# Performance work log

Hardware: AMD Instinct MI355X
Metric: run time of the kernel (lower is better)

Reference implementation:

```python
import jax, jax.numpy as jnp
import numpy as np
from jax import lax

B, T, D, U = 64, 512, 1024, 1024
INIT_SCALE = 0.05  # keras 'uniform' initializer: U(-0.05, 0.05)


def setup_inputs() -> dict:
    key = jax.random.key(0)
    kx, kw, ku = jax.random.split(key, 3)
    x = jax.random.normal(kx, (B, T, D), dtype=jnp.float32)
    kernel = jax.random.uniform(kw, (D, U), dtype=jnp.float32,
                                minval=-INIT_SCALE, maxval=INIT_SCALE)
    recurrent_kernel = jax.random.uniform(ku, (U, U), dtype=jnp.float32,
                                          minval=-INIT_SCALE, maxval=INIT_SCALE)
    return {"x": x, "kernel": kernel, "recurrent_kernel": recurrent_kernel}


def reference(x, kernel, recurrent_kernel):
    # h_t = x_t @ W + h_{t-1} @ U, h_0 = 0; return last h (return_sequences=False)
    # Precompute the input projection for all timesteps in one big GEMM.
    xs = jnp.einsum('btd,du->btu', x, kernel)          # [B, T, U]
    h0 = jnp.zeros((x.shape[0], recurrent_kernel.shape[0]), dtype=x.dtype)

    def step(h, xt):
        h = xt + h @ recurrent_kernel                   # [B, U]
        return h, None

    h_last, _ = lax.scan(step, h0, jnp.swapaxes(xs, 0, 1))  # scan over T
    return h_last                                       # [B, U]
```

## Files before the change

### kernel.cpp

```cpp
#include <hip/hip_runtime.h>
#include <hip/hip_bf16.h>

typedef __attribute__((ext_vector_type(4))) float f32x4;
typedef __attribute__((ext_vector_type(8))) short bf16x8;
typedef __attribute__((ext_vector_type(4))) short s16x4;

#define SLOT (1024 * 1024)

__device__ __forceinline__ short f2bfs(float f) {
  __hip_bfloat16 h = __float2bfloat16(f);
  union { __hip_bfloat16 h; short s; } u; u.h = h;
  return u.s;
}
__device__ __forceinline__ float bf2fs(short s) {
  union { unsigned u; float f; } v; v.u = ((unsigned)(unsigned short)s) << 16;
  return v.f;
}

__device__ __forceinline__ void gload16(void* l, const void* g) {
  __builtin_amdgcn_global_load_lds(
      (const __attribute__((address_space(1))) unsigned int*)g,
      (__attribute__((address_space(3))) unsigned int*)l, 16, 0, 0);
}

template<int RM>
__device__ __forceinline__ int rmap(int R) {
  return (RM == 0) ? R
       : (RM == 3) ? (((R & 63) << 9) | ((R >> 6) << 2))
                   : (((R >> 6) << 7) | (R & 63));
}

template<int ADD, int OUT>
__device__ __forceinline__ void epi128(
    f32x4 (&acc)[4][4], void* __restrict__ Cp, int ldc,
    const short* __restrict__ AddP,
    int row0, int col0, int M, int wave, int lane) {
  const int wm = wave >> 1, wn = wave & 1;
  const int l16 = lane & 15;
  #pragma unroll
  for (int m = 0; m < 4; ++m) {
    #pragma unroll
    for (int n = 0; n < 4; ++n) {
      const int grow0 = row0 + wm * 64 + m * 16 + ((lane >> 4) << 2);
      const int gcol  = col0 + wn * 64 + n * 16 + l16;
      #pragma unroll
      for (int r = 0; r < 4; ++r) {
        const int R = grow0 + r;
        if (R < M) {
          float val = acc[m][n][r];
          if (ADD == 2) {
            int ar = (((R >> 6) << 7) | (R & 63)) + 64;
            val += bf2fs(AddP[(size_t)ar * 1024 + gcol]);
          }
          if (OUT == 0) ((short*)Cp)[(size_t)R * ldc + gcol] = f2bfs(val);
          else          ((float*)Cp)[(size_t)R * ldc + gcol] = val;
        }
      }
    }
  }
}

struct TileAddr {
  const short *a0, *a1, *b0, *b1;
  int dA0, dA1, dB0, dB1;
  int offA[4], offB[4];
};
template<int RM>
__device__ __forceinline__ TileAddr mk_addr(
    const short* A, int lda, const short* BT, int ldb,
    int row0, int col0, int tid, int wave, int lane) {
  TileAddr t;
  const int wm = wave >> 1, wn = wave & 1;
  const int l16 = lane & 15, kg = lane >> 4;
  const int r0 = tid >> 2, g0 = tid & 3;
  const int gs0 = g0 ^ ((r0 >> 1) & 3);
  const int r1 = r0 + 64;
  const int gs1 = g0 ^ ((r1 >> 1) & 3);
  t.a0 = A + (size_t)rmap<RM>(row0 + r0) * lda + gs0 * 8;
  t.a1 = A + (size_t)rmap<RM>(row0 + r1) * lda + gs1 * 8;
  t.b0 = BT + (size_t)(col0 + r0) * ldb + gs0 * 8;
  t.b1 = BT + (size_t)(col0 + r1) * ldb + gs1 * 8;
  t.dA0 = tid * 16; t.dA1 = t.dA0 + 4096;
  t.dB0 = 8192 + tid * 16; t.dB1 = t.dB0 + 4096;
  #pragma unroll
  for (int m = 0; m < 4; ++m) {
    int row = wm * 64 + m * 16 + l16;
    t.offA[m] = (row * 4 + (kg ^ ((row >> 1) & 3))) * 16;
  }
  #pragma unroll
  for (int n = 0; n < 4; ++n) {
    int c = wn * 64 + n * 16 + l16;
    t.offB[n] = 8192 + (c * 4 + (kg ^ ((c >> 1) & 3))) * 16;
  }
  return t;
}
__device__ __forceinline__ void stage_to(const TileAddr& ta, char* buf, int ko) {
  gload16(buf + ta.dA0, ta.a0 + ko); gload16(buf + ta.dA1, ta.a1 + ko);
  gload16(buf + ta.dB0, ta.b0 + ko); gload16(buf + ta.dB1, ta.b1 + ko);
}
__device__ __forceinline__ void compute_step(
    const TileAddr& ta, const char* buf, f32x4 (&acc)[4][4]) {
  bf16x8 af[4], bfr[4];
  #pragma unroll
  for (int m = 0; m < 4; ++m) af[m] = *(const bf16x8*)(buf + ta.offA[m]);
  #pragma unroll
  for (int n = 0; n < 4; ++n) bfr[n] = *(const bf16x8*)(buf + ta.offB[n]);
  __builtin_amdgcn_s_setprio(1);
  #pragma unroll
  for (int m = 0; m < 4; ++m)
    #pragma unroll
    for (int n = 0; n < 4; ++n)
      acc[m][n] = __builtin_amdgcn_mfma_f32_16x16x32_bf16(af[m], bfr[n], acc[m][n], 0, 0, 0);
  __builtin_amdgcn_s_setprio(0);
}
template<int RM>
__device__ __forceinline__ void gemm128_d4(
    char* lds, f32x4 (&acc)[4][4],
    const short* __restrict__ A, int lda,
    const short* __restrict__ BT, int ldb,
    int row0, int col0, int nkt, int tid, int wave, int lane) {
  TileAddr ta = mk_addr<RM>(A, lda, BT, ldb, row0, col0, tid, wave, lane);
  #pragma unroll
  for (int p = 0; p < 4; ++p)
    stage_to(ta, lds + p * 16384, p * 32);
  int bufc = 0, bufn = 4;
  for (int t = 0; t < nkt; ++t) {
    const int w = nkt - 1 - t;
    if (w >= 3)      { asm volatile("s_waitcnt vmcnt(12)" ::: "memory"); }
    else if (w == 2) { asm volatile("s_waitcnt vmcnt(8)" ::: "memory"); }
    else if (w == 1) { asm volatile("s_waitcnt vmcnt(4)" ::: "memory"); }
    else             { asm volatile("s_waitcnt vmcnt(0)" ::: "memory"); }
    __builtin_amdgcn_s_barrier();
    asm volatile("" ::: "memory");
    if (t + 4 < nkt) stage_to(ta, lds + bufn * 16384, (t + 4) * 32);
    compute_step(ta, lds + bufc * 16384, acc);
    bufc = (bufc == 4) ? 0 : bufc + 1;
    bufn = (bufn == 4) ? 0 : bufn + 1;
  }
}
__device__ __forceinline__ void run_unit_d4(char* lds,
    const short* A, const short* BT, short* C, int ldc,
    int tile, int tid, int wave, int lane) {
  f32x4 acc[4][4] = {};
  int row0 = (tile >> 3) * 128, col0 = (tile & 7) * 128;
  gemm128_d4<0>(lds, acc, A, 1024, BT, 1024, row0, col0, 32, tid, wave, lane);
  epi128<0, 0>(acc, C, ldc, nullptr, row0, col0, 1024, wave, lane);
}

template<int RM>
__device__ __forceinline__ void gemm8ph(
    char* lds, f32x4 (&acc)[4][4],
    const short* __restrict__ A, int lda,
    const short* __restrict__ BT, int ldb,
    int row0, int col0, int nkt, int tid, int wave, int lane) {
  const int wm = wave >> 1, wn = wave & 1;
  const int l16 = lane & 15, kg = (lane >> 4) & 3;

  const short* aP[2][2];
  #pragma unroll
  for (int l = 0; l < 2; ++l) {
    int G = l * 512 + tid;
    int rp = G >> 3, gs = (G & 7) ^ (rp & 7);
    #pragma unroll
    for (int h = 0; h < 2; ++h)
      aP[l][h] = A + (size_t)rmap<RM>(row0 + h * 128 + rp) * lda + gs * 8;
  }
  const short* bP[2];
  {
    int rp = tid >> 3, gs = (tid & 7) ^ (rp & 7);
    #pragma unroll
    for (int h = 0; h < 2; ++h)
      bP[h] = BT + (size_t)(col0 + h * 64 + rp) * ldb + gs * 8;
  }

  int offA[4][2], offB[4][2];
  #pragma unroll
  for (int m = 0; m < 4; ++m) {
    int rp = (wm & 1) * 64 + m * 16 + l16;
    #pragma unroll
    for (int ks = 0; ks < 2; ++ks) {
      int gsrc = ks * 4 + kg;
      offA[m][ks] = (wm >> 1) * 16384 + (rp * 8 + (gsrc ^ (rp & 7))) * 16;
    }
  }
  #pragma unroll
  for (int n = 0; n < 4; ++n) {
    int rp = n * 16 + l16;
    #pragma unroll
    for (int ks = 0; ks < 2; ++ks) {
      int gsrc = ks * 4 + kg;
      offB[n][ks] = wn * 8192 + (rp * 8 + (gsrc ^ (rp & 7))) * 16;
    }
  }

  auto SA = [&](int kt, int ad_t, int h) {
    char* dst = lds + ad_t * 32768 + h * 16384 + tid * 16;
    gload16(dst,        aP[0][h] + kt * 64);
    gload16(dst + 8192, aP[1][h] + kt * 64);
  };
  auto SB = [&](int kt, int h) {
    gload16(lds + 98304 + (kt & 1) * 16384 + h * 8192 + tid * 16,
            bP[h] + kt * 64);
  };

  SA(0, 0, 0); SA(0, 0, 1);
  SB(0, 0); SB(0, 1);
  SA(1, 1, 0); SA(1, 1, 1);
  SB(1, 0); SB(1, 1);

  bf16x8 bR[4][2];
  int ad = 0;
  for (int kt = 0; kt < nkt; ++kt) {
    char* baseA = lds + ad * 32768;
    char* baseB = lds + 98304 + (kt & 1) * 16384;
    const int ad2 = (ad >= 1) ? ad - 1 : 2;
    if (kt == nkt - 1) { asm volatile("s_waitcnt vmcnt(0)" ::: "memory"); }
    else               { asm volatile("s_waitcnt vmcnt(6)" ::: "memory"); }
    __builtin_amdgcn_s_barrier();
    __builtin_amdgcn_sched_barrier(0);
    {
      #pragma unroll
      for (int n = 0; n < 4; ++n)
        #pragma unroll
        for (int ks = 0; ks < 2; ++ks)
          bR[n][ks] = *(const bf16x8*)(baseB + offB[n][ks]);
      bf16x8 aR[2][2];
      #pragma unroll
      for (int mm = 0; mm < 2; ++mm)
        #pragma unroll
        for (int ks = 0; ks < 2; ++ks)
          aR[mm][ks] = *(const bf16x8*)(baseA + offA[mm][ks]);
      if (kt + 2 < nkt) { SA(kt + 2, ad2, 0); SA(kt + 2, ad2, 1); }
      __builtin_amdgcn_s_setprio(1);
      #pragma unroll
      for (int mm = 0; mm < 2; ++mm)
        #pragma unroll
        for (int n = 0; n < 4; ++n)
          #pragma unroll
          for (int ks = 0; ks < 2; ++ks)
            acc[mm][n] = __builtin_amdgcn_mfma_f32_16x16x32_bf16(
                aR[mm][ks], bR[n][ks], acc[mm][n], 0, 0, 0);
      __builtin_amdgcn_s_setprio(0);
    }
    __builtin_amdgcn_s_barrier();
    __builtin_amdgcn_sched_barrier(0);
    {
      bf16x8 aR[2][2];
      #pragma unroll
      for (int mm = 0; mm < 2; ++mm)
        #pragma unroll
        for (int ks = 0; ks < 2; ++ks)
          aR[mm][ks] = *(const bf16x8*)(baseA + offA[2 + mm][ks]);
      if (kt + 2 < nkt) { SB(kt + 2, 0); SB(kt + 2, 1); }
      __builtin_amdgcn_s_setprio(1);
      #pragma unroll
      for (int mm = 0; mm < 2; ++mm)
        #pragma unroll
        for (int n = 0; n < 4; ++n)
          #pragma unroll
          for (int ks = 0; ks < 2; ++ks)
            acc[2 + mm][n] = __builtin_amdgcn_mfma_f32_16x16x32_bf16(
                aR[mm][ks], bR[n][ks], acc[2 + mm][n], 0, 0, 0);
      __builtin_amdgcn_s_setprio(0);
    }
    ad = (ad == 2) ? 0 : ad + 1;
  }
}

__device__ __forceinline__ void run_unit8(char* lds,
    const short* A, const short* BT, short* C, int ldc,
    int tile, int tid, int wave, int lane) {
  f32x4 acc[4][4] = {};
  int row0 = (tile >> 3) * 256, col0 = (tile & 7) * 128;
  gemm8ph<0>(lds, acc, A, 1024, BT, 1024, row0, col0, 16, tid, wave, lane);
  epi128<0, 0>(acc, C, ldc, nullptr, row0, col0, 1024, wave, lane);
}


__global__ __launch_bounds__(256) void k_prep(
    const float* __restrict__ W, const float* __restrict__ Uf,
    const float* __restrict__ X,
    short* __restrict__ BTcat, short* __restrict__ slab, short* __restrict__ XB) {
  __shared__ float tf[32][36];
  int b = blockIdx.x, t = threadIdx.x;
  if (b < 2048) {
    const float* src = (b < 1024) ? W : Uf;
    int bb = b & 1023;
    int i0 = (bb >> 5) * 32, j0 = (bb & 31) * 32;
    int r = t >> 3, c = (t & 7) * 4;
    *(f32x4*)&tf[r][c] = *(const f32x4*)(src + (size_t)(i0 + r) * 1024 + j0 + c);
    __syncthreads();
    s16x4 o;
    o.x = f2bfs(tf[c + 0][r]); o.y = f2bfs(tf[c + 1][r]);
    o.z = f2bfs(tf[c + 2][r]); o.w = f2bfs(tf[c + 3][r]);
    if (b < 1024)
      *(s16x4*)(BTcat + (size_t)(j0 + r) * 4096 + 3072 + i0 + c) = o;
    else
      *(s16x4*)(slab + (size_t)(j0 + r) * 1024 + i0 + c) = o;
  } else if (b < 3072) {
    int q = b - 2048;
    const float* src = (q < 512) ? Uf : W;
    short* dst = slab + (size_t)((q < 512) ? 9 : 17) * SLOT;
    int qq = q & 511;
    size_t base = (size_t)qq * 2048 + (size_t)t * 8;
    f32x4 a = *(const f32x4*)(src + base);
    f32x4 c2 = *(const f32x4*)(src + base + 4);
    bf16x8 o;
    o[0] = f2bfs(a.x);  o[1] = f2bfs(a.y);  o[2] = f2bfs(a.z);  o[3] = f2bfs(a.w);
    o[4] = f2bfs(c2.x); o[5] = f2bfs(c2.y); o[6] = f2bfs(c2.z); o[7] = f2bfs(c2.w);
    *(bf16x8*)(dst + base) = o;
  } else {
    int q = b - 3072;
    size_t base = ((size_t)q * 256 + t) * 32;
    #pragma unroll
    for (int i = 0; i < 4; ++i) {
      f32x4 a = *(const f32x4*)(X + base + i * 8);
      f32x4 c2 = *(const f32x4*)(X + base + i * 8 + 4);
      bf16x8 o;
      o[0] = f2bfs(a.x);  o[1] = f2bfs(a.y);  o[2] = f2bfs(a.z);  o[3] = f2bfs(a.w);
      o[4] = f2bfs(c2.x); o[5] = f2bfs(c2.y); o[6] = f2bfs(c2.z); o[7] = f2bfs(c2.w);
      *(bf16x8*)(XB + base + i * 8) = o;
    }
  }
}

__global__ __launch_bounds__(512) void k_pre1(short* slab, short* BTcat) {
  __shared__ __align__(16) char lds[131072];
  int tid = threadIdx.x, wave = tid >> 6, lane = tid & 63;
  int b = blockIdx.x, u = b >> 5, q = b & 31;
  short* s = slab;
  if (u == 0)
    run_unit8(lds, s, s + (size_t)9 * SLOT, s + (size_t)1 * SLOT, 1024, q, tid, wave, lane);
  else if (u == 1)
    run_unit8(lds, s + (size_t)9 * SLOT, s, s + (size_t)10 * SLOT, 1024, q, tid, wave, lane);
  else if (u == 2)
    run_unit8(lds, s, s + (size_t)17 * SLOT, BTcat + 2048, 4096, q, tid, wave, lane);
  else
    run_unit8(lds, s + (size_t)17 * SLOT, s, s + (size_t)16 * SLOT, 1024, q, tid, wave, lane);
}

__global__ __launch_bounds__(512) void k_pre2(short* slab, short* BTcat) {
  __shared__ __align__(16) char lds[131072];
  int tid = threadIdx.x, wave = tid >> 6, lane = tid & 63;
  int b = blockIdx.x, u = b >> 5, q = b & 31;
  short* s = slab;
  if (u == 0)
    run_unit8(lds, s + (size_t)1 * SLOT, s + (size_t)17 * SLOT, BTcat + 1024, 4096, q, tid, wave, lane);
  else if (u == 1)
    run_unit8(lds, s + (size_t)1 * SLOT, s + (size_t)16 * SLOT, BTcat, 4096, q, tid, wave, lane);
  else if (u == 2)
    run_unit8(lds, s + (size_t)1 * SLOT, s + (size_t)10 * SLOT, s + (size_t)2 * SLOT, 1024, q, tid, wave, lane);
  else
    run_unit8(lds, s + (size_t)10 * SLOT, s + (size_t)1 * SLOT, s + (size_t)11 * SLOT, 1024, q, tid, wave, lane);
}

__global__ __launch_bounds__(512) void k_big(
    const short* __restrict__ XB, const short* __restrict__ BTcat,
    short* __restrict__ FA) {
  __shared__ __align__(16) char lds[131072];
  int tid = threadIdx.x, wave = tid >> 6, lane = tid & 63;
  int c = blockIdx.x;
  int c2 = (c & 7) * 32 + (c >> 3);
  f32x4 acc[4][4] = {};
  int row0 = (c2 >> 3) * 256, col0 = (c2 & 7) * 128;
  gemm8ph<3>(lds, acc, XB, 1024, BTcat, 4096, row0, col0, 64, tid, wave, lane);
  epi128<0, 0>(acc, FA, 1024, nullptr, row0, col0, 8192, wave, lane);
}

template<int OUT>
__global__ __launch_bounds__(256) void k_lvl(
    const short* __restrict__ Fin, const short* __restrict__ PT,
    void* __restrict__ Fout, int M, int nComb,
    const short* __restrict__ sA0, const short* __restrict__ sB0, short* __restrict__ sC0,
    const short* __restrict__ sA1, const short* __restrict__ sB1, short* __restrict__ sC1) {
  __shared__ __align__(16) char lds[81920];
  int tid = threadIdx.x, wave = tid >> 6, lane = tid & 63;
  int b = blockIdx.x;
  if (b < nComb) {
    f32x4 acc[4][4] = {};
    int row0 = (b >> 3) * 128, col0 = (b & 7) * 128;
    gemm128_d4<2>(lds, acc, Fin, 1024, PT, 1024, row0, col0, 32, tid, wave, lane);
    epi128<2, OUT>(acc, Fout, 1024, Fin, row0, col0, M, wave, lane);
  } else {
    int q = b - nComb;
    const short* sa = (q < 64) ? sA0 : sA1;
    const short* sb = (q < 64) ? sB0 : sB1;
    short* sc = (q < 64) ? sC0 : sC1;
    run_unit_d4(lds, sa, sb, sc, 1024, q & 63, tid, wave, lane);
  }
}

extern "C" void kernel_launch(void* const* d_in, const int* in_sizes, int n_in,
                              void* d_out, int out_size, void* d_ws, size_t ws_size,
                              hipStream_t stream) {
  const float* X = (const float*)d_in[0];
  const float* W = (const float*)d_in[1];
  const float* U = (const float*)d_in[2];
  float* outp = (float*)d_out;

  char* ws = (char*)d_ws;
  short* XB    = (short*)ws;
  short* FB    = (short*)ws;
  short* BTcat = (short*)(ws + ((size_t)64 << 20));
  short* slab  = (short*)(ws + ((size_t)72 << 20));
  short* FA    = (short*)(ws + ((size_t)108 << 20));
  auto sl = [&](int i) { return slab + (size_t)i * SLOT; };

  k_prep<<<7168, 256, 0, stream>>>(W, U, X, BTcat, slab, XB);
  k_pre1<<<128, 512, 0, stream>>>(slab, BTcat);
  k_pre2<<<128, 512, 0, stream>>>(slab, BTcat);
  k_big<<<256, 512, 0, stream>>>(XB, BTcat, FA);

  k_lvl<0><<<384, 256, 0, stream>>>(FA, sl(2), FB, 4096, 256,
                                    sl(2), sl(11), sl(3), sl(11), sl(2), sl(12));
  k_lvl<0><<<256, 256, 0, stream>>>(FB, sl(3), FA, 2048, 128,
                                    sl(3), sl(12), sl(4), sl(12), sl(3), sl(13));
  k_lvl<0><<<192, 256, 0, stream>>>(FA, sl(4), FB, 1024, 64,
                                    sl(4), sl(13), sl(5), sl(13), sl(4), sl(14));
  k_lvl<0><<<160, 256, 0, stream>>>(FB, sl(5), FA, 512, 32,
                                    sl(5), sl(14), sl(6), sl(14), sl(5), sl(15));
  k_lvl<0><<<144, 256, 0, stream>>>(FA, sl(6), FB, 256, 16,
                                    sl(6), sl(15), sl(7), sl(15), sl(6), sl(16));
  k_lvl<0><<<72, 256, 0, stream>>>(FB, sl(7), FA, 128, 8,
                                   sl(7), sl(16), sl(8), nullptr, nullptr, nullptr);
  k_lvl<1><<<8, 256, 0, stream>>>(FA, sl(8), outp, 64, 8,
                                  nullptr, nullptr, nullptr, nullptr, nullptr, nullptr);
}
```

Baseline: 320.0 us.

## Overlap X bf16 conversion with small weight-power GEMMs in fused kernels

Takes the fp32-to-bf16 conversion of the large input X out of the prep kernel. It splits that work across the two small precompute GEMM launches, which before used only 128 workgroups. Extra workgroups in each launch now convert half of X, so the bandwidth-bound conversion runs beside the compute-bound weight-power GEMMs. The cost is a heavier launch of 2176 blocks, each needing 128KB of LDS because the GEMM and convert blocks share one kernel. This can limit how many convert blocks fit per CU and can delay the GEMM blocks.

```diff
diff --git a/kernel.cpp b/kernel.cpp
--- a/kernel.cpp
+++ b/kernel.cpp
@@ -277,10 +277,9 @@
 }
 
 
-__global__ __launch_bounds__(256) void k_prep(
+__global__ __launch_bounds__(256) void k_prep_tc(
     const float* __restrict__ W, const float* __restrict__ Uf,
-    const float* __restrict__ X,
-    short* __restrict__ BTcat, short* __restrict__ slab, short* __restrict__ XB) {
+    short* __restrict__ BTcat, short* __restrict__ slab) {
   __shared__ float tf[32][36];
   int b = blockIdx.x, t = threadIdx.x;
   if (b < 2048) {
@@ -297,7 +296,7 @@
       *(s16x4*)(BTcat + (size_t)(j0 + r) * 4096 + 3072 + i0 + c) = o;
     else
       *(s16x4*)(slab + (size_t)(j0 + r) * 1024 + i0 + c) = o;
-  } else if (b < 3072) {
+  } else {
     int q = b - 2048;
     const float* src = (q < 512) ? Uf : W;
     short* dst = slab + (size_t)((q < 512) ? 9 : 17) * SLOT;
@@ -309,49 +308,50 @@
     o[0] = f2bfs(a.x);  o[1] = f2bfs(a.y);  o[2] = f2bfs(a.z);  o[3] = f2bfs(a.w);
     o[4] = f2bfs(c2.x); o[5] = f2bfs(c2.y); o[6] = f2bfs(c2.z); o[7] = f2bfs(c2.w);
     *(bf16x8*)(dst + base) = o;
+  }
+}
+
+template<int PH>
+__global__ __launch_bounds__(512) void k_fuse(
+    const float* __restrict__ X, short* __restrict__ XB,
+    short* slab, short* BTcat) {
+  __shared__ __align__(16) char lds[131072];
+  int tid = threadIdx.x;
+  int b = blockIdx.x;
+  short* s = slab;
+  if (b < 128) {
+    int wave = tid >> 6, lane = tid & 63;
+    int u = b >> 5, q = b & 31;
+    if (PH == 0) {
+      if (u == 0)
+        run_unit8(lds, s, s + (size_t)9 * SLOT, s + (size_t)1 * SLOT, 1024, q, tid, wave, lane);
+      else if (u == 1)
+        run_unit8(lds, s + (size_t)9 * SLOT, s, s + (size_t)10 * SLOT, 1024, q, tid, wave, lane);
+      else if (u == 2)
+        run_unit8(lds, s, s + (size_t)17 * SLOT, BTcat + 2048, 4096, q, tid, wave, lane);
+      else
+        run_unit8(lds, s + (size_t)17 * SLOT, s, s + (size_t)16 * SLOT, 1024, q, tid, wave, lane);
+    } else {
+      if (u == 0)
+        run_unit8(lds, s + (size_t)1 * SLOT, s + (size_t)17 * SLOT, BTcat + 1024, 4096, q, tid, wave, lane);
+      else if (u == 1)
+        run_unit8(lds, s + (size_t)1 * SLOT, s + (size_t)16 * SLOT, BTcat, 4096, q, tid, wave, lane);
+      else if (u == 2)
+        run_unit8(lds, s + (size_t)1 * SLOT, s + (size_t)10 * SLOT, s + (size_t)2 * SLOT, 1024, q, tid, wave, lane);
+      else
+        run_unit8(lds, s + (size_t)10 * SLOT, s + (size_t)1 * SLOT, s + (size_t)11 * SLOT, 1024, q, tid, wave, lane);
+    }
   } else {
-    int q = b - 3072;
-    size_t base = ((size_t)q * 256 + t) * 32;
+    size_t base = ((size_t)(b - 128 + PH * 2048)) * 8192;
     #pragma unroll
     for (int i = 0; i < 4; ++i) {
-      f32x4 a = *(const f32x4*)(X + base + i * 8);
-      f32x4 c2 = *(const f32x4*)(X + base + i * 8 + 4);
-      bf16x8 o;
-      o[0] = f2bfs(a.x);  o[1] = f2bfs(a.y);  o[2] = f2bfs(a.z);  o[3] = f2bfs(a.w);
-      o[4] = f2bfs(c2.x); o[5] = f2bfs(c2.y); o[6] = f2bfs(c2.z); o[7] = f2bfs(c2.w);
-      *(bf16x8*)(XB + base + i * 8) = o;
-    }
-  }
-}
-
-__global__ __launch_bounds__(512) void k_pre1(short* slab, short* BTcat) {
-  __shared__ __align__(16) char lds[131072];
-  int tid = threadIdx.x, wave = tid >> 6, lane = tid & 63;
-  int b = blockIdx.x, u = b >> 5, q = b & 31;
-  short* s = slab;
-  if (u == 0)
-    run_unit8(lds, s, s + (size_t)9 * SLOT, s + (size_t)1 * SLOT, 1024, q, tid, wave, lane);
-  else if (u == 1)
-    run_unit8(lds, s + (size_t)9 * SLOT, s, s + (size_t)10 * SLOT, 1024, q, tid, wave, lane);
-  else if (u == 2)
-    run_unit8(lds, s, s + (size_t)17 * SLOT, BTcat + 2048, 4096, q, tid, wave, lane);
-  else
-    run_unit8(lds, s + (size_t)17 * SLOT, s, s + (size_t)16 * SLOT, 1024, q, tid, wave, lane);
-}
-
-__global__ __launch_bounds__(512) void k_pre2(short* slab, short* BTcat) {
-  __shared__ __align__(16) char lds[131072];
-  int tid = threadIdx.x, wave = tid >> 6, lane = tid & 63;
-  int b = blockIdx.x, u = b >> 5, q = b & 31;
-  short* s = slab;
-  if (u == 0)
-    run_unit8(lds, s + (size_t)1 * SLOT, s + (size_t)17 * SLOT, BTcat + 1024, 4096, q, tid, wave, lane);
-  else if (u == 1)
-    run_unit8(lds, s + (size_t)1 * SLOT, s + (size_t)16 * SLOT, BTcat, 4096, q, tid, wave, lane);
-  else if (u == 2)
-    run_unit8(lds, s + (size_t)1 * SLOT, s + (size_t)10 * SLOT, s + (size_t)2 * SLOT, 1024, q, tid, wave, lane);
-  else
-    run_unit8(lds, s + (size_t)10 * SLOT, s + (size_t)1 * SLOT, s + (size_t)11 * SLOT, 1024, q, tid, wave, lane);
+      size_t idx = base + (size_t)i * 2048 + (size_t)tid * 4;
+      f32x4 v = *(const f32x4*)(X + idx);
+      s16x4 o;
+      o.x = f2bfs(v.x); o.y = f2bfs(v.y); o.z = f2bfs(v.z); o.w = f2bfs(v.w);
+      *(s16x4*)(XB + idx) = o;
+    }
+  }
 }
 
 __global__ __launch_bounds__(512) void k_big(
@@ -406,9 +406,9 @@
   short* FA    = (short*)(ws + ((size_t)108 << 20));
   auto sl = [&](int i) { return slab + (size_t)i * SLOT; };
 
-  k_prep<<<7168, 256, 0, stream>>>(W, U, X, BTcat, slab, XB);
-  k_pre1<<<128, 512, 0, stream>>>(slab, BTcat);
-  k_pre2<<<128, 512, 0, stream>>>(slab, BTcat);
+  k_prep_tc<<<3072, 256, 0, stream>>>(W, U, BTcat, slab);
+  k_fuse<0><<<2176, 512, 0, stream>>>(X, XB, slab, BTcat);
+  k_fuse<1><<<2176, 512, 0, stream>>>(X, XB, slab, BTcat);
   k_big<<<256, 512, 0, stream>>>(XB, BTcat, FA);
 
   k_lvl<0><<<384, 256, 0, stream>>>(FA, sl(2), FB, 4096, 256,
```

Result: faster. 299.8 us (median of 2 runs) (-6.3%).
